# Kernel tuning notes

Hardware: AMD Instinct MI355X
Metric: run time of the kernel (lower is better)

## Reference

```python
import jax, jax.numpy as jnp
import numpy as np

E, B, T, N, DIN = 8, 1024, 64, 16, 8
H, Z = 512, 128
DFLAT = T * N * DIN  # 8192


def setup_inputs() -> dict:
    key = jax.random.key(0)
    ks = jax.random.split(key, 10)
    def w(k, shape, fan_in):
        return jax.random.normal(k, shape, jnp.float32) * (1.0 / np.sqrt(fan_in))
    return {
        'x': jax.random.normal(ks[0], (B, T, N, DIN), jnp.float32),
        'eps': jax.random.normal(ks[1], (E, B, Z), jnp.float32),
        'enc_w1': w(ks[2], (E, DFLAT, H), DFLAT), 'enc_b1': jnp.zeros((E, H), jnp.float32),
        'enc_w2': w(ks[3], (E, H, H), H),         'enc_b2': jnp.zeros((E, H), jnp.float32),
        'mu_w':   w(ks[4], (E, H, Z), H),         'mu_b':   jnp.zeros((E, Z), jnp.float32),
        'lv_w':   w(ks[5], (E, H, Z), H),         'lv_b':   jnp.zeros((E, Z), jnp.float32),
        'dec_w1': w(ks[6], (E, Z, H), Z),         'dec_b1': jnp.zeros((E, H), jnp.float32),
        'dec_w2': w(ks[7], (E, H, H), H),         'dec_b2': jnp.zeros((E, H), jnp.float32),
        'dec_w3': w(ks[8], (E, H, DFLAT), H),     'dec_b3': jnp.zeros((E, DFLAT), jnp.float32),
    }


def _all_experts(x, eps, enc_w1, enc_b1, enc_w2, enc_b2, mu_w, mu_b, lv_w, lv_b,
                 dec_w1, dec_b1, dec_w2, dec_b2, dec_w3, dec_b3):
    # 'everyone_try_this_problem': every expert runs densely on the full batch.
    xf = x.reshape(x.shape[0], -1)                                            # [B, D]
    h = jax.nn.relu(jnp.einsum('bd,edh->ebh', xf, enc_w1) + enc_b1[:, None])  # [E, B, H]
    h = jax.nn.relu(jnp.einsum('ebh,ehk->ebk', h, enc_w2) + enc_b2[:, None])
    mu = jnp.einsum('ebh,ehz->ebz', h, mu_w) + mu_b[:, None]                  # [E, B, Z]
    logvar = jnp.einsum('ebh,ehz->ebz', h, lv_w) + lv_b[:, None]
    z = mu + jnp.exp(0.5 * logvar) * eps                                      # reparameterized sample
    hd = jax.nn.relu(jnp.einsum('ebz,ezh->ebh', z, dec_w1) + dec_b1[:, None])
    hd = jax.nn.relu(jnp.einsum('ebh,ehk->ebk', hd, dec_w2) + dec_b2[:, None])
    xhat = jnp.einsum('ebh,ehd->ebd', hd, dec_w3) + dec_b3[:, None]           # [E, B, D]
    losses = jnp.mean((xhat - xf[None]) ** 2, axis=-1)                        # [E, B] per-sample recon loss
    return mu, logvar, xhat, losses


def reference(x, eps, enc_w1, enc_b1, enc_w2, enc_b2, mu_w, mu_b, lv_w, lv_b,
              dec_w1, dec_b1, dec_w2, dec_b2, dec_w3, dec_b3):
    mu, logvar, xhat, losses = _all_experts(
        x, eps, enc_w1, enc_b1, enc_w2, enc_b2, mu_w, mu_b, lv_w, lv_b,
        dec_w1, dec_b1, dec_w2, dec_b2, dec_w3, dec_b3)
    # torch.min(all_loss[B,E], dim=1) -> argmin over experts (first-index tiebreak)
    expert_idx = jnp.argmin(losses, axis=0)                                   # [B]
    b = jnp.arange(x.shape[0])
    mu_sel = mu[expert_idx, b]                                                # [B, Z]
    logvar_sel = logvar[expert_idx, b]
    xhat_sel = xhat[expert_idx, b].reshape(x.shape)                           # [B, T, N, DIN]
    return mu_sel, logvar_sel, xhat_sel, expert_idx
```

## Files before the change

kernel.cpp:

```cpp
#include <hip/hip_runtime.h>

#define EE 8
#define BB 1024
#define DD 8192
#define HH 512
#define ZZ 128

typedef __attribute__((ext_vector_type(8))) short bf16x8;
typedef __attribute__((ext_vector_type(4))) float f32x4;
typedef __attribute__((address_space(1))) unsigned int u32g;
typedef __attribute__((address_space(3))) unsigned int u32l;

#define DEVI __device__ __forceinline__

DEVI float4 ld4(const float* p) { return *(const float4*)p; }

DEVI unsigned f2bf_u(float x) {
  unsigned u = __builtin_bit_cast(unsigned, x);
  return (u + 0x7FFFu + ((u >> 16) & 1u)) >> 16;
}
DEVI float bfu2f(unsigned h) { return __builtin_bit_cast(float, h << 16); }
DEVI float bf2f(short s) {
  return __builtin_bit_cast(float, ((unsigned)(unsigned short)s) << 16);
}
DEVI void split2(float x, short& hi, short& lo) {
  unsigned h = f2bf_u(x);
  hi = (short)h;
  lo = (short)f2bf_u(x - bfu2f(h));
}

DEVI void gload16(const void* g, void* l) {
  __builtin_amdgcn_global_load_lds((const u32g*)g, (u32l*)l, 16, 0, 0);
}

DEVI void pipe_fence() {
  __builtin_amdgcn_sched_barrier(0);
  asm volatile("s_waitcnt vmcnt(0)" ::: "memory");
  __builtin_amdgcn_s_barrier();
  __builtin_amdgcn_sched_barrier(0);
}

template <int ROWS, int WAVES>
DEVI void stageG(const short* src, int Kb, short* lds, int w, int laneoff) {
  const char* p = (const char*)src + laneoff;
  char* l = (char*)lds + w * 1024;
#pragma unroll
  for (int r = 0; r < ROWS / (WAVES * 8); ++r)
    gload16(p + (size_t)r * (WAVES * 8) * Kb, l + r * (WAVES * 1024));
}

template <int ROWS, int WAVES>
DEVI void stage32(const short* src, int Kb, short* lds, int w, int laneoff32) {
  const char* p = (const char*)src + laneoff32;
  char* l = (char*)lds + w * 1024;
#pragma unroll
  for (int r = 0; r < ROWS / (WAVES * 16); ++r)
    gload16(p + (size_t)r * (WAVES * 16) * Kb, l + r * (WAVES * 1024));
}

template <int NPASS, int NF>
DEVI void mma_chunk(const char* Ah, const char* Al, const char* Bh, const char* Bl,
                    int abase, int bbase, f32x4 acc[4][NF]) {
#pragma unroll
  for (int kk = 0; kk < 2; ++kk) {
    const int kx = kk * 64;
    bf16x8 ah[4], al[4], bh[NF], bl[NF];
#pragma unroll
    for (int m = 0; m < 4; ++m) {
      ah[m] = *(const bf16x8*)(Ah + ((abase + m * 2048) ^ kx));
      if (NPASS == 3) al[m] = *(const bf16x8*)(Al + ((abase + m * 2048) ^ kx));
    }
#pragma unroll
    for (int n = 0; n < NF; ++n) {
      bh[n] = *(const bf16x8*)(Bh + ((bbase + n * 2048) ^ kx));
      if (NPASS == 3) bl[n] = *(const bf16x8*)(Bl + ((bbase + n * 2048) ^ kx));
    }
#pragma unroll
    for (int m = 0; m < 4; ++m)
#pragma unroll
      for (int n = 0; n < NF; ++n) {
        acc[m][n] = __builtin_amdgcn_mfma_f32_16x16x32_bf16(ah[m], bh[n], acc[m][n], 0, 0, 0);
        if (NPASS == 3) {
          acc[m][n] = __builtin_amdgcn_mfma_f32_16x16x32_bf16(ah[m], bl[n], acc[m][n], 0, 0, 0);
          acc[m][n] = __builtin_amdgcn_mfma_f32_16x16x32_bf16(al[m], bh[n], acc[m][n], 0, 0, 0);
        }
      }
  }
}

template <int NM, int NF>
DEVI void mma32(const char* A, const char* B, int abase, int bbase,
                f32x4 acc[NM][NF]) {
  bf16x8 ah[NM], bh[NF];
#pragma unroll
  for (int m = 0; m < NM; ++m) ah[m] = *(const bf16x8*)(A + abase + m * 1024);
#pragma unroll
  for (int n = 0; n < NF; ++n) bh[n] = *(const bf16x8*)(B + bbase + n * 1024);
#pragma unroll
  for (int m = 0; m < NM; ++m)
#pragma unroll
    for (int n = 0; n < NF; ++n)
      acc[m][n] = __builtin_amdgcn_mfma_f32_16x16x32_bf16(ah[m], bh[n], acc[m][n], 0, 0, 0);
}

template <int NPASS, int NF, bool RELU, int OUT>
__global__ __launch_bounds__(256, (NPASS == 3 ? 2 : 3)) void gemm_k(
    const short* __restrict__ Ahg, const short* __restrict__ Alg,
    const short* __restrict__ Bhg, const short* __restrict__ Blg,
    const float* __restrict__ bias,
    float* __restrict__ Yf, short* __restrict__ Yh, short* __restrict__ Yl,
    int M, int N, int K, int APE, const int* __restrict__ cntPtr, int mSkip) {
  constexpr int BN = NF * 32;
  __shared__ short sA[(NPASS == 3 ? 2 : 1) * 128 * 64];
  __shared__ short sB[(NPASS == 3 ? 2 : 1) * BN * 64];
  const int e = blockIdx.z;
  const int m0 = blockIdx.y * 128, n0 = blockIdx.x * BN;
  if (m0 < mSkip) return;
  if (cntPtr) {
    if (m0 >= ((cntPtr[0] + 127) & ~127)) return;
  }
  const size_t eA = APE ? (size_t)e * M * K : 0;
  const short* Ae = Ahg + eA + (size_t)m0 * K;
  const short* Ale = (NPASS == 3) ? (Alg + eA + (size_t)m0 * K) : nullptr;
  const short* Be = Bhg + ((size_t)e * N + n0) * K;
  const short* Ble = (NPASS == 3) ? (Blg + ((size_t)e * N + n0) * K) : nullptr;

  const int t = threadIdx.x, w = t >> 6, lane = t & 63;
  const int wm = w >> 1, wn = w & 1;
  const int Kb = K * 2;
  const int laneoff = (w * 8 + (lane >> 3)) * Kb + (((lane & 7) ^ ((lane >> 3) & 7)) << 4);
  const int r16 = lane & 15, g = lane >> 4;
  const int c0 = ((g ^ (r16 & 7)) << 4);
  const int abase = (wm * 64 + r16) * 128 + c0;
  const int bbase = (wn * (NF * 16) + r16) * 128 + c0;

  f32x4 acc[4][NF];
#pragma unroll
  for (int m = 0; m < 4; ++m)
#pragma unroll
    for (int n = 0; n < NF; ++n) acc[m][n] = (f32x4){0.f, 0.f, 0.f, 0.f};

  for (int k0 = 0; k0 < K; k0 += 64) {
    stageG<128, 4>(Ae + k0, Kb, sA, w, laneoff);
    if (NPASS == 3) stageG<128, 4>(Ale + k0, Kb, sA + 128 * 64, w, laneoff);
    stageG<BN, 4>(Be + k0, Kb, sB, w, laneoff);
    if (NPASS == 3) stageG<BN, 4>(Ble + k0, Kb, sB + BN * 64, w, laneoff);
    __syncthreads();
    mma_chunk<NPASS, NF>((const char*)sA, (const char*)(sA + 128 * 64),
                         (const char*)sB, (const char*)(sB + BN * 64), abase, bbase, acc);
    __syncthreads();
  }

  const int col0 = n0 + wn * (NF * 16);
#pragma unroll
  for (int n = 0; n < NF; ++n) {
    const int cn = col0 + n * 16 + r16;
    const float bv = bias[(size_t)e * N + cn];
#pragma unroll
    for (int m = 0; m < 4; ++m)
#pragma unroll
      for (int r = 0; r < 4; ++r) {
        const int row = m0 + wm * 64 + m * 16 + g * 4 + r;
        float v = acc[m][n][r] + bv;
        if (RELU) v = fmaxf(v, 0.f);
        const size_t o = ((size_t)e * M + row) * N + cn;
        if (OUT == 0) {
          Yf[o] = v;
        } else {
          unsigned hb = f2bf_u(v);
          Yh[o] = (short)hb;
          if (NPASS == 3) Yl[o] = (short)f2bf_u(v - bfu2f(hb));
        }
      }
  }
}

__global__ __launch_bounds__(256, 4) void enc1_mainsplit_k(
    const short* __restrict__ Xhg, const short* __restrict__ Bhg,
    float* __restrict__ EncP) {
  __shared__ short sA[2][128 * 32];
  __shared__ short sB[2][64 * 32];
  const int raw = blockIdx.x;
  const int e = raw & 7;
  const int q = raw >> 3;
  const int m0 = (q & 7) * 128;
  const int ks = (q >> 3) & 1;
  const int n0 = (q >> 4) * 64;
  const int Kb = DD * 2;
  const short* Ae = Xhg + (size_t)m0 * DD;
  const short* Be = Bhg + ((size_t)e * HH + n0) * DD;

  const int t = threadIdx.x, w = t >> 6, lane = t & 63;
  const int wm = w >> 1, wn = w & 1;
  const int lo32 = (w * 16 + (lane >> 2)) * Kb +
                   (((lane & 3) ^ ((lane >> 3) & 3)) << 4);
  const int r16 = lane & 15, g = lane >> 4;
  const int c32 = (g ^ ((r16 >> 1) & 3)) << 4;
  const int abase = (wm * 64 + r16) * 64 + c32;
  const int bbase = (wn * 32 + r16) * 64 + c32;

  f32x4 acc[4][2];
#pragma unroll
  for (int m = 0; m < 4; ++m)
#pragma unroll
    for (int n = 0; n < 2; ++n) acc[m][n] = (f32x4){0.f, 0.f, 0.f, 0.f};

  const int kbeg = ks * 4096;
  stage32<128, 4>(Ae + kbeg, Kb, sA[0], w, lo32);
  stage32<64, 4>(Be + kbeg, Kb, sB[0], w, lo32);
  pipe_fence();
  for (int c = 0; c < 128; c += 2) {
    if (c + 1 < 128) {
      stage32<128, 4>(Ae + kbeg + (c + 1) * 32, Kb, sA[1], w, lo32);
      stage32<64, 4>(Be + kbeg + (c + 1) * 32, Kb, sB[1], w, lo32);
    }
    mma32<4, 2>((const char*)sA[0], (const char*)sB[0], abase, bbase, acc);
    pipe_fence();
    if (c + 2 < 128) {
      stage32<128, 4>(Ae + kbeg + (c + 2) * 32, Kb, sA[0], w, lo32);
      stage32<64, 4>(Be + kbeg + (c + 2) * 32, Kb, sB[0], w, lo32);
    }
    mma32<4, 2>((const char*)sA[1], (const char*)sB[1], abase, bbase, acc);
    pipe_fence();
  }

#pragma unroll
  for (int n = 0; n < 2; ++n) {
    const int cn = n0 + wn * 32 + n * 16 + r16;
#pragma unroll
    for (int m = 0; m < 4; ++m)
#pragma unroll
      for (int r = 0; r < 4; ++r) {
        const int row = m0 + wm * 64 + m * 16 + g * 4 + r;
        EncP[(((size_t)ks * EE + e) * BB + row) * HH + cn] = acc[m][n][r];
      }
  }
}

__global__ void fuse_enc1main_k(const float* __restrict__ EncP,
                                const float* __restrict__ enc_b1,
                                short* __restrict__ Hh) {
  const int idx = blockIdx.x * 256 + threadIdx.x;
  const size_t base = (size_t)idx * 8;
  float s[8];
  *(float4*)&s[0] = *(const float4*)&EncP[base];
  *(float4*)&s[4] = *(const float4*)&EncP[base + 4];
  {
    const float* p = EncP + (size_t)(EE * BB * HH) + base;
    float q[8];
    *(float4*)&q[0] = *(const float4*)p;
    *(float4*)&q[4] = *(const float4*)(p + 4);
#pragma unroll
    for (int j = 0; j < 8; ++j) s[j] += q[j];
  }
  const int e = (int)(base / (BB * HH));
  const int col = (int)(base % HH);
  short h8[8];
#pragma unroll
  for (int j = 0; j < 8; ++j) {
    const float v = fmaxf(s[j] + enc_b1[e * HH + col + j], 0.f);
    h8[j] = (short)f2bf_u(v);
  }
  *(bf16x8*)&Hh[base] = *(bf16x8*)h8;
}

__global__ __launch_bounds__(512, 2) void gemm_loss256_k(
    const short* __restrict__ Ahg, const short* __restrict__ Bhg,
    const float* __restrict__ bias, const short* __restrict__ xfh,
    float* __restrict__ partials) {
  __shared__ short sA[2][256 * 32];
  __shared__ short sB[2][256 * 32];
  __shared__ float red[256][4];
  int lin = blockIdx.x + 32 * (blockIdx.y + 4 * blockIdx.z);
  lin = (lin & 7) * 128 + (lin >> 3);
  const int bx = lin & 31, by = (lin >> 5) & 3, e = lin >> 7;
  const int m0 = by * 256, n0 = bx * 256;
  const int Kb = HH * 2;
  const short* Ae = Ahg + ((size_t)e * BB + m0) * HH;
  const short* Be = Bhg + ((size_t)e * DD + n0) * HH;

  const int t = threadIdx.x, w = t >> 6, lane = t & 63;
  const int wm = w >> 2, wn = w & 3;
  const int lo32 = (w * 16 + (lane >> 2)) * Kb +
                   (((lane & 3) ^ ((lane >> 3) & 3)) << 4);
  const int r16 = lane & 15, g = lane >> 4;
  const int c32 = (g ^ ((r16 >> 1) & 3)) << 4;
  const int abase = (wm * 128 + r16) * 64 + c32;
  const int bbase = (wn * 64 + r16) * 64 + c32;

  f32x4 acc[8][4];
#pragma unroll
  for (int m = 0; m < 8; ++m)
#pragma unroll
    for (int n = 0; n < 4; ++n) acc[m][n] = (f32x4){0.f, 0.f, 0.f, 0.f};

  stage32<256, 8>(Ae, Kb, sA[0], w, lo32);
  stage32<256, 8>(Be, Kb, sB[0], w, lo32);
  pipe_fence();
  for (int c = 0; c < 16; c += 2) {
    if (c + 1 < 16) {
      stage32<256, 8>(Ae + (c + 1) * 32, Kb, sA[1], w, lo32);
      stage32<256, 8>(Be + (c + 1) * 32, Kb, sB[1], w, lo32);
    }
    mma32<8, 4>((const char*)sA[0], (const char*)sB[0], abase, bbase, acc);
    pipe_fence();
    if (c + 2 < 16) {
      stage32<256, 8>(Ae + (c + 2) * 32, Kb, sA[0], w, lo32);
      stage32<256, 8>(Be + (c + 2) * 32, Kb, sB[0], w, lo32);
    }
    mma32<8, 4>((const char*)sA[1], (const char*)sB[1], abase, bbase, acc);
    pipe_fence();
  }

  float rs[8][4];
#pragma unroll
  for (int m = 0; m < 8; ++m)
#pragma unroll
    for (int r = 0; r < 4; ++r) rs[m][r] = 0.f;
#pragma unroll
  for (int n = 0; n < 4; ++n) {
    const int cn = n0 + wn * 64 + n * 16 + r16;
    const float bv = bias[(size_t)e * DD + cn];
#pragma unroll
    for (int m = 0; m < 8; ++m)
#pragma unroll
      for (int r = 0; r < 4; ++r) {
        const int row = m0 + wm * 128 + m * 16 + g * 4 + r;
        const float d = acc[m][n][r] + bv - bf2f(xfh[(size_t)row * DD + cn]);
        rs[m][r] = fmaf(d, d, rs[m][r]);
      }
  }
#pragma unroll
  for (int off = 1; off < 16; off <<= 1)
#pragma unroll
    for (int m = 0; m < 8; ++m)
#pragma unroll
      for (int r = 0; r < 4; ++r) rs[m][r] += __shfl_xor(rs[m][r], off);
  if (r16 == 0) {
#pragma unroll
    for (int m = 0; m < 8; ++m)
#pragma unroll
      for (int r = 0; r < 4; ++r) red[wm * 128 + m * 16 + g * 4 + r][wn] = rs[m][r];
  }
  __syncthreads();
  if (t < 256)
    partials[((size_t)e * BB + m0 + t) * 32 + bx] =
        red[t][0] + red[t][1] + red[t][2] + red[t][3];
}

template <int NPASS>
__global__ __launch_bounds__(256, 2) void gemm_loss_k(
    const short* __restrict__ Ahg, const short* __restrict__ Alg,
    const short* __restrict__ Bhg, const short* __restrict__ Blg,
    const float* __restrict__ bias, const float* __restrict__ xf,
    const int* __restrict__ rows, const int* __restrict__ cntPtr,
    float* __restrict__ partials, int K) {
  constexpr int NF = 4;
  __shared__ short sA[2 * 128 * 64];
  __shared__ short sB[2 * 128 * 64];
  __shared__ float red[128][2];
  const int e = blockIdx.z;
  const int m0 = blockIdx.y * 128, n0 = blockIdx.x * 128;
  int cntA = BB;
  if (cntPtr) {
    cntA = cntPtr[0];
    if (m0 >= ((cntA + 127) & ~127)) return;
  }
  const short* Ae = Ahg + ((size_t)e * BB + m0) * K;
  const short* Ale = Alg + ((size_t)e * BB + m0) * K;
  const short* Be = Bhg + ((size_t)e * DD + n0) * K;
  const short* Ble = Blg + ((size_t)e * DD + n0) * K;

  const int t = threadIdx.x, w = t >> 6, lane = t & 63;
  const int wm = w >> 1, wn = w & 1;
  const int Kb = K * 2;
  const int laneoff = (w * 8 + (lane >> 3)) * Kb + (((lane & 7) ^ ((lane >> 3) & 7)) << 4);
  const int r16 = lane & 15, g = lane >> 4;
  const int c0 = ((g ^ (r16 & 7)) << 4);
  const int abase = (wm * 64 + r16) * 128 + c0;
  const int bbase = (wn * 64 + r16) * 128 + c0;

  f32x4 acc[4][NF];
#pragma unroll
  for (int m = 0; m < 4; ++m)
#pragma unroll
    for (int n = 0; n < NF; ++n) acc[m][n] = (f32x4){0.f, 0.f, 0.f, 0.f};

  for (int k0 = 0; k0 < K; k0 += 64) {
    stageG<128, 4>(Ae + k0, Kb, sA, w, laneoff);
    stageG<128, 4>(Ale + k0, Kb, sA + 128 * 64, w, laneoff);
    stageG<128, 4>(Be + k0, Kb, sB, w, laneoff);
    stageG<128, 4>(Ble + k0, Kb, sB + 128 * 64, w, laneoff);
    __syncthreads();
    mma_chunk<NPASS, NF>((const char*)sA, (const char*)(sA + 128 * 64),
                         (const char*)sB, (const char*)(sB + 128 * 64), abase, bbase, acc);
    __syncthreads();
  }

  float rs[4][4];
#pragma unroll
  for (int m = 0; m < 4; ++m)
#pragma unroll
    for (int r = 0; r < 4; ++r) rs[m][r] = 0.f;
#pragma unroll
  for (int n = 0; n < NF; ++n) {
    const int cn = n0 + wn * 64 + n * 16 + r16;
    const float bv = bias[(size_t)e * DD + cn];
#pragma unroll
    for (int m = 0; m < 4; ++m)
#pragma unroll
      for (int r = 0; r < 4; ++r) {
        const int lrow = m0 + wm * 64 + m * 16 + g * 4 + r;
        const int xr = rows ? (lrow < cntA ? rows[lrow] : 0) : lrow;
        const float d = acc[m][n][r] + bv - xf[(size_t)xr * DD + cn];
        rs[m][r] = fmaf(d, d, rs[m][r]);
      }
  }
#pragma unroll
  for (int off = 1; off < 16; off <<= 1)
#pragma unroll
    for (int m = 0; m < 4; ++m)
#pragma unroll
      for (int r = 0; r < 4; ++r) rs[m][r] += __shfl_xor(rs[m][r], off);
  if (r16 == 0) {
#pragma unroll
    for (int m = 0; m < 4; ++m)
#pragma unroll
      for (int r = 0; r < 4; ++r) red[wm * 64 + m * 16 + g * 4 + r][wn] = rs[m][r];
  }
  __syncthreads();
  if (t < 128)
    partials[((size_t)e * BB + m0 + t) * 64 + blockIdx.x] = red[t][0] + red[t][1];
}

__global__ __launch_bounds__(512, 2) void gather_out256_k(
    const short* __restrict__ Ahg, const short* __restrict__ Bhg,
    const float* __restrict__ bias, const int* __restrict__ counts,
    const int* __restrict__ lists, float* __restrict__ out) {
  __shared__ short sA[2][256 * 32];
  __shared__ short sB[2][256 * 32];
  __shared__ int rows_s[256];
  const int e = blockIdx.z;
  const int cnt = counts[e];
  const int m0 = blockIdx.y * 256;
  if (m0 >= cnt) return;
  const int n0 = blockIdx.x * 256;
  const int Kb = HH * 2;
  const short* Ae = Ahg + (size_t)e * BB * HH;
  const short* Be = Bhg + ((size_t)e * DD + n0) * HH;

  const int t = threadIdx.x, w = t >> 6, lane = t & 63;
  const int wm = w >> 2, wn = w & 3;
  const int soff = ((lane & 3) ^ ((lane >> 3) & 3)) << 4;
  const int lo32 = (w * 16 + (lane >> 2)) * Kb + soff;
  const int r16 = lane & 15, g = lane >> 4;
  const int c32 = (g ^ ((r16 >> 1) & 3)) << 4;
  const int abase = (wm * 128 + r16) * 64 + c32;
  const int bbase = (wn * 64 + r16) * 64 + c32;

  if (t < 256) rows_s[t] = (m0 + t < cnt) ? lists[e * BB + m0 + t] : -1;
  __syncthreads();
  const int r1 = w * 16 + (lane >> 2), r2 = r1 + 128;
  int g1 = rows_s[r1]; g1 = g1 < 0 ? 0 : g1;
  int g2 = rows_s[r2]; g2 = g2 < 0 ? 0 : g2;

  f32x4 acc[8][4];
#pragma unroll
  for (int m = 0; m < 8; ++m)
#pragma unroll
    for (int n = 0; n < 4; ++n) acc[m][n] = (f32x4){0.f, 0.f, 0.f, 0.f};

  auto STAGE_A = [&](int ke, short* dst) {
    gload16((const char*)Ae + (size_t)g1 * Kb + (size_t)ke * 2 + soff,
            (char*)dst + w * 1024);
    gload16((const char*)Ae + (size_t)g2 * Kb + (size_t)ke * 2 + soff,
            (char*)dst + 8192 + w * 1024);
  };

  STAGE_A(0, sA[0]);
  stage32<256, 8>(Be, Kb, sB[0], w, lo32);
  pipe_fence();
  for (int c = 0; c < 16; c += 2) {
    if (c + 1 < 16) {
      STAGE_A((c + 1) * 32, sA[1]);
      stage32<256, 8>(Be + (c + 1) * 32, Kb, sB[1], w, lo32);
    }
    mma32<8, 4>((const char*)sA[0], (const char*)sB[0], abase, bbase, acc);
    pipe_fence();
    if (c + 2 < 16) {
      STAGE_A((c + 2) * 32, sA[0]);
      stage32<256, 8>(Be + (c + 2) * 32, Kb, sB[0], w, lo32);
    }
    mma32<8, 4>((const char*)sA[1], (const char*)sB[1], abase, bbase, acc);
    pipe_fence();
  }

#pragma unroll
  for (int n = 0; n < 4; ++n) {
    const int cn = n0 + wn * 64 + n * 16 + r16;
    const float bv = bias[(size_t)e * DD + cn];
#pragma unroll
    for (int m = 0; m < 8; ++m)
#pragma unroll
      for (int r = 0; r < 4; ++r) {
        const int rout = rows_s[wm * 128 + m * 16 + g * 4 + r];
        if (rout >= 0) out[(size_t)rout * DD + cn] = acc[m][n][r] + bv;
      }
  }
}

__global__ __launch_bounds__(256, 2) void enc1_pksplit_k(
    const short* __restrict__ Ahg, const short* __restrict__ Alg,
    const short* __restrict__ Bhg, const short* __restrict__ Blg,
    const int* __restrict__ cntPtr, float* __restrict__ PAf) {
  __shared__ short sA[2 * 128 * 64];
  __shared__ short sB[2 * 64 * 64];
  const int cnt = cntPtr[0];
  if (cnt == 0) return;
  const int m0 = blockIdx.y * 128;
  if (m0 >= ((cnt + 127) & ~127)) return;
  const int e = blockIdx.z;
  const int n0 = (blockIdx.x & 7) * 64;
  const int ks = blockIdx.x >> 3;
  const int Kb = DD * 2;
  const short* Ae = Ahg + (size_t)m0 * DD;
  const short* Ale = Alg + (size_t)m0 * DD;
  const short* Be = Bhg + ((size_t)e * HH + n0) * DD;
  const short* Ble = Blg + ((size_t)e * HH + n0) * DD;

  const int t = threadIdx.x, w = t >> 6, lane = t & 63;
  const int wm = w >> 1, wn = w & 1;
  const int laneoff = (w * 8 + (lane >> 3)) * Kb + (((lane & 7) ^ ((lane >> 3) & 7)) << 4);
  const int r16 = lane & 15, g = lane >> 4;
  const int c0 = ((g ^ (r16 & 7)) << 4);
  const int abase = (wm * 64 + r16) * 128 + c0;
  const int bbase = (wn * 32 + r16) * 128 + c0;

  f32x4 acc[4][2];
#pragma unroll
  for (int m = 0; m < 4; ++m)
#pragma unroll
    for (int n = 0; n < 2; ++n) acc[m][n] = (f32x4){0.f, 0.f, 0.f, 0.f};

  const int kbeg = ks * 1024, kend = kbeg + 1024;
  for (int k0 = kbeg; k0 < kend; k0 += 64) {
    stageG<128, 4>(Ae + k0, Kb, sA, w, laneoff);
    stageG<128, 4>(Ale + k0, Kb, sA + 128 * 64, w, laneoff);
    stageG<64, 4>(Be + k0, Kb, sB, w, laneoff);
    stageG<64, 4>(Ble + k0, Kb, sB + 64 * 64, w, laneoff);
    __syncthreads();
    mma_chunk<3, 2>((const char*)sA, (const char*)(sA + 128 * 64),
                    (const char*)sB, (const char*)(sB + 64 * 64), abase, bbase, acc);
    __syncthreads();
  }

#pragma unroll
  for (int n = 0; n < 2; ++n) {
    const int cn = n0 + wn * 32 + n * 16 + r16;
#pragma unroll
    for (int m = 0; m < 4; ++m)
#pragma unroll
      for (int r = 0; r < 4; ++r) {
        const int row = m0 + wm * 64 + m * 16 + g * 4 + r;
        PAf[(((size_t)ks * EE + e) * 256 + row) * HH + cn] = acc[m][n][r];
      }
  }
}

__global__ void fuse_enc1_k(const float* __restrict__ PAf,
                            const float* __restrict__ enc_b1,
                            const int* __restrict__ ambc,
                            short* __restrict__ PAh, short* __restrict__ PAl) {
  const int cnt = ambc[0];
  if (cnt == 0) return;
  const int cntPad = (cnt + 127) & ~127;
  const int idx = blockIdx.x * 256 + threadIdx.x;
  const size_t base = (size_t)idx * 8;
  const int e = (int)(base / (256 * HH));
  const int rem = (int)(base % (256 * HH));
  const int row = rem / HH;
  if (row >= cntPad) return;
  const int col = rem % HH;
  const size_t src = ((size_t)e * 256 + row) * HH + col;
  float s[8];
  *(float4*)&s[0] = *(const float4*)&PAf[src];
  *(float4*)&s[4] = *(const float4*)&PAf[src + 4];
#pragma unroll
  for (int ks = 1; ks < 8; ++ks) {
    const float* p = PAf + (size_t)ks * (EE * 256 * HH) + src;
    float q[8];
    *(float4*)&q[0] = *(const float4*)p;
    *(float4*)&q[4] = *(const float4*)(p + 4);
#pragma unroll
    for (int j = 0; j < 8; ++j) s[j] += q[j];
  }
  short h8[8], l8[8];
#pragma unroll
  for (int j = 0; j < 8; ++j) {
    const float v = fmaxf(s[j] + enc_b1[e * HH + col + j], 0.f);
    split2(v, h8[j], l8[j]);
  }
  const size_t o = ((size_t)e * BB + row) * HH + col;
  *(bf16x8*)&PAh[o] = *(bf16x8*)h8;
  *(bf16x8*)&PAl[o] = *(bf16x8*)l8;
}

__global__ void init_k(int* ambc) { ambc[0] = 0; }

__global__ void split_x_k(const float* __restrict__ x, short* __restrict__ Xh) {
  const int i = (blockIdx.x * 256 + threadIdx.x) * 8;
  float v[8];
  *(float4*)&v[0] = ld4(x + i);
  *(float4*)&v[4] = ld4(x + i + 4);
  short h[8];
#pragma unroll
  for (int j = 0; j < 8; ++j) h[j] = (short)f2bf_u(v[j]);
  *(bf16x8*)&Xh[i] = *(bf16x8*)h;
}

__global__ void biascat_k(const float* __restrict__ mu_b, const float* __restrict__ lv_b,
                          float* __restrict__ mlvB) {
  const int e = blockIdx.x, t = threadIdx.x;
  mlvB[e * 256 + t] = t < 128 ? mu_b[e * 128 + t] : lv_b[e * 128 + t - 128];
}

__global__ __launch_bounds__(256) void trans_split_k(
    const float* __restrict__ W, short* __restrict__ Th, short* __restrict__ Tl,
    int K, int N, int rowOff, int rowsPerE) {
  const int e = blockIdx.z;
  const int k0 = blockIdx.x * 64, n0 = blockIdx.y * 64;
  __shared__ float tile[64][65];
  const int t = threadIdx.x;
  const int tr = t >> 2, tc = (t & 3) * 16;
  const float* Wp = W + ((size_t)e * K + k0 + tr) * N + n0 + tc;
#pragma unroll
  for (int c = 0; c < 4; ++c) {
    float4 v = *(const float4*)(Wp + c * 4);
    tile[tr][tc + c * 4 + 0] = v.x;
    tile[tr][tc + c * 4 + 1] = v.y;
    tile[tr][tc + c * 4 + 2] = v.z;
    tile[tr][tc + c * 4 + 3] = v.w;
  }
  __syncthreads();
  short h8[16], l8[16];
#pragma unroll
  for (int j = 0; j < 16; ++j) split2(tile[tc + j][tr], h8[j], l8[j]);
  const size_t o = ((size_t)e * rowsPerE + rowOff + n0 + tr) * K + k0 + tc;
  *(bf16x8*)&Th[o] = *(bf16x8*)&h8[0];
  *(bf16x8*)&Th[o + 8] = *(bf16x8*)&h8[8];
  *(bf16x8*)&Tl[o] = *(bf16x8*)&l8[0];
  *(bf16x8*)&Tl[o + 8] = *(bf16x8*)&l8[8];
}

__global__ void z_k(const float* __restrict__ mlv, const float* __restrict__ eps,
                    short* __restrict__ Zh) {
  const int t = blockIdx.x * 256 + threadIdx.x;
  const int eb = t >> 7, z = t & 127;
  const float mu = mlv[(size_t)eb * 256 + z], lv = mlv[(size_t)eb * 256 + 128 + z];
  Zh[t] = (short)f2bf_u(fmaf(expf(0.5f * lv), eps[t], mu));
}

__global__ void zP_k(const float* __restrict__ mlvP, const float* __restrict__ eps,
                     const int* __restrict__ ambc, const int* __restrict__ amb,
                     short* __restrict__ ZgH, short* __restrict__ ZgL) {
  const int t = blockIdx.x * 256 + threadIdx.x;
  const int eb = t >> 7, z = t & 127;
  const int e = eb >> 10, i = eb & 1023;
  const int cntA = ambc[0];
  if (i >= ((cntA + 127) & ~127)) return;
  const int b = (i < cntA) ? amb[i] : 0;
  const float mu = mlvP[(size_t)eb * 256 + z], lv = mlvP[(size_t)eb * 256 + 128 + z];
  const float v = fmaf(expf(0.5f * lv), eps[((size_t)e * BB + b) * ZZ + z], mu);
  short h, l;
  split2(v, h, l);
  ZgH[t] = h;
  ZgL[t] = l;
}

__global__ void gather_x_k(const float* __restrict__ x, const int* __restrict__ ambc,
                           const int* __restrict__ amb, short* __restrict__ XgH,
                           short* __restrict__ XgL) {
  const int i = blockIdx.x;
  const int cntA = ambc[0];
  if (i >= ((cntA + 127) & ~127)) return;
  const int b = (i < cntA) ? amb[i] : 0;
  const float* xr = x + (size_t)b * DD;
  short* oh = XgH + (size_t)i * DD;
  short* ol = XgL + (size_t)i * DD;
  for (int j = threadIdx.x * 8; j < DD; j += 256 * 8) {
    float v[8];
    *(float4*)&v[0] = ld4(xr + j);
    *(float4*)&v[4] = ld4(xr + j + 4);
    short h[8], l[8];
#pragma unroll
    for (int q = 0; q < 8; ++q) split2(v[q], h[q], l[q]);
    *(bf16x8*)&oh[j] = *(bf16x8*)h;
    *(bf16x8*)&ol[j] = *(bf16x8*)l;
  }
}

__global__ void loss_reduce_k(const float* __restrict__ part, float* __restrict__ loss,
                              const int* __restrict__ cntPtr, int NBLK) {
  const int id = blockIdx.x * 256 + threadIdx.x;
  if (cntPtr) {
    if ((id & 1023) >= ((cntPtr[0] + 127) & ~127)) return;
  }
  const float* p = part + (size_t)id * NBLK;
  float s = 0.f;
  for (int j = 0; j < NBLK; ++j) s += p[j];
  loss[id] = s;
}

__global__ void argmin_flag_k(const float* __restrict__ loss, int* __restrict__ idx,
                              float* __restrict__ out_ix, int* __restrict__ ambc,
                              int* __restrict__ amb) {
  const int b = blockIdx.x * 256 + threadIdx.x;
  float best = loss[b], sec = 3.0e38f;
  int bi = 0;
#pragma unroll
  for (int e = 1; e < EE; ++e) {
    const float v = loss[e * BB + b];
    if (v < best) { sec = best; best = v; bi = e; }
    else if (v < sec) sec = v;
  }
  idx[b] = bi;
  out_ix[b] = (float)bi;
  if (sec - best < 10.0f + 0.001f * best) {
    int p = atomicAdd(ambc, 1);
    amb[p] = b;
  }
}

__global__ void fix_idx_k(const float* __restrict__ lossP, const int* __restrict__ ambc,
                          const int* __restrict__ amb, int* __restrict__ idx,
                          float* __restrict__ out_ix) {
  const int i = blockIdx.x * 256 + threadIdx.x;
  if (i >= ambc[0]) return;
  const int b = amb[i];
  float best = lossP[i];
  int bi = 0;
#pragma unroll
  for (int e = 1; e < EE; ++e) {
    const float v = lossP[e * 1024 + i];
    if (v < best) { best = v; bi = e; }
  }
  idx[b] = bi;
  out_ix[b] = (float)bi;
}

__global__ void select_k(const float* __restrict__ mlv, const int* __restrict__ idx,
                         float* __restrict__ out_mu, float* __restrict__ out_lv) {
  const int t = blockIdx.x * 256 + threadIdx.x;
  const int b = t >> 7, z = t & 127;
  const int e = idx[b];
  out_mu[t] = mlv[((size_t)(e * BB + b)) * 256 + z];
  out_lv[t] = mlv[((size_t)(e * BB + b)) * 256 + 128 + z];
}

__global__ void compact_k(const int* __restrict__ idx, int* __restrict__ counts,
                          int* __restrict__ lists) {
  __shared__ int cnt[EE];
  if (threadIdx.x < EE) cnt[threadIdx.x] = 0;
  __syncthreads();
  const int b = threadIdx.x;
  const int e = idx[b];
  const int pos = atomicAdd(&cnt[e], 1);
  lists[e * BB + pos] = b;
  __syncthreads();
  if (threadIdx.x < EE) counts[threadIdx.x] = cnt[threadIdx.x];
}

extern "C" void kernel_launch(void* const* d_in, const int* in_sizes, int n_in,
                              void* d_out, int out_size, void* d_ws, size_t ws_size,
                              hipStream_t stream) {
  const float* x      = (const float*)d_in[0];
  const float* eps    = (const float*)d_in[1];
  const float* enc_w1 = (const float*)d_in[2];
  const float* enc_b1 = (const float*)d_in[3];
  const float* enc_w2 = (const float*)d_in[4];
  const float* enc_b2 = (const float*)d_in[5];
  const float* mu_w   = (const float*)d_in[6];
  const float* mu_b   = (const float*)d_in[7];
  const float* lv_w   = (const float*)d_in[8];
  const float* lv_b   = (const float*)d_in[9];
  const float* dec_w1 = (const float*)d_in[10];
  const float* dec_b1 = (const float*)d_in[11];
  const float* dec_w2 = (const float*)d_in[12];
  const float* dec_b2 = (const float*)d_in[13];
  const float* dec_w3 = (const float*)d_in[14];
  const float* dec_b3 = (const float*)d_in[15];

  char* wsb = (char*)d_ws;
  size_t off = 0;
  auto alloc = [&](size_t bytes) -> void* {
    void* p = wsb + off;
    off = (off + bytes + 511) & ~(size_t)511;
    return p;
  };
  short* Xh    = (short*)alloc(16777216);
  short* ew1Th = (short*)alloc(67108864);
  short* ew1Tl = (short*)alloc(67108864);
  short* ew2Th = (short*)alloc(4194304);
  short* ew2Tl = (short*)alloc(4194304);
  short* mlvTh = (short*)alloc(2097152);
  short* mlvTl = (short*)alloc(2097152);
  short* dw1Th = (short*)alloc(1048576);
  short* dw1Tl = (short*)alloc(1048576);
  short* dw2Th = (short*)alloc(4194304);
  short* dw2Tl = (short*)alloc(4194304);
  short* dw3Th = (short*)alloc(67108864);
  short* dw3Tl = (short*)alloc(67108864);
  short* Hh    = (short*)alloc(8388608);
  short* H2h   = (short*)alloc(8388608);
  float* mlv   = (float*)alloc(8388608);
  float* mlvB  = (float*)alloc(8192);
  short* Zh    = (short*)alloc(2097152);
  float* part  = (float*)alloc(2097152);
  float* loss  = (float*)alloc(32768);
  int*   idx   = (int*)alloc(4096);
  int*   ambc  = (int*)alloc(512);
  int*   amb   = (int*)alloc(4096);
  int*   counts= (int*)alloc(512);
  int*   lists = (int*)alloc(4096);
  short* XgL   = (short*)alloc(16777216);
  short* PAh   = (short*)alloc(8388608);
  short* PAl   = (short*)alloc(8388608);
  short* PBh   = (short*)alloc(8388608);
  short* PBl   = (short*)alloc(8388608);
  float* mlvP  = (float*)alloc(8388608);
  short* ZgH   = (short*)alloc(2097152);
  short* ZgL   = (short*)alloc(2097152);
  float* lossP = (float*)alloc(32768);
  float* PAf   = (float*)alloc(33554432);
  short* XgH   = Xh;
  float* EncP  = (float*)XgL;

  float* out_mu = (float*)d_out;
  float* out_lv = out_mu + (size_t)BB * ZZ;
  float* out_xh = out_lv + (size_t)BB * ZZ;
  float* out_ix = out_xh + (size_t)BB * DD;

  const dim3 blk(256);

  init_k<<<1, 1, 0, stream>>>(ambc);
  split_x_k<<<4096, blk, 0, stream>>>(x, Xh);
  biascat_k<<<8, blk, 0, stream>>>(mu_b, lv_b, mlvB);
  trans_split_k<<<dim3(128, 8, 8), blk, 0, stream>>>(enc_w1, ew1Th, ew1Tl, 8192, 512, 0, 512);
  trans_split_k<<<dim3(8, 8, 8), blk, 0, stream>>>(enc_w2, ew2Th, ew2Tl, 512, 512, 0, 512);
  trans_split_k<<<dim3(8, 2, 8), blk, 0, stream>>>(mu_w, mlvTh, mlvTl, 512, 128, 0, 256);
  trans_split_k<<<dim3(8, 2, 8), blk, 0, stream>>>(lv_w, mlvTh, mlvTl, 512, 128, 128, 256);
  trans_split_k<<<dim3(2, 8, 8), blk, 0, stream>>>(dec_w1, dw1Th, dw1Tl, 128, 512, 0, 512);
  trans_split_k<<<dim3(8, 8, 8), blk, 0, stream>>>(dec_w2, dw2Th, dw2Tl, 512, 512, 0, 512);
  trans_split_k<<<dim3(8, 128, 8), blk, 0, stream>>>(dec_w3, dw3Th, dw3Tl, 512, 8192, 0, 8192);

  enc1_mainsplit_k<<<dim3(1024), blk, 0, stream>>>(Xh, ew1Th, EncP);
  fuse_enc1main_k<<<2048, blk, 0, stream>>>(EncP, enc_b1, Hh);
  gemm_k<1, 2, true, 1><<<dim3(8, 8, 8), blk, 0, stream>>>(
      Hh, nullptr, ew2Th, nullptr, enc_b2, nullptr, H2h, nullptr, 1024, 512, 512, 1, nullptr, 0);
  gemm_k<1, 2, false, 0><<<dim3(4, 8, 8), blk, 0, stream>>>(
      H2h, nullptr, mlvTh, nullptr, mlvB, mlv, nullptr, nullptr, 1024, 256, 512, 1, nullptr, 0);
  z_k<<<4096, blk, 0, stream>>>(mlv, eps, Zh);
  gemm_k<1, 2, true, 1><<<dim3(8, 8, 8), blk, 0, stream>>>(
      Zh, nullptr, dw1Th, nullptr, dec_b1, nullptr, Hh, nullptr, 1024, 512, 128, 1, nullptr, 0);
  gemm_k<1, 2, true, 1><<<dim3(8, 8, 8), blk, 0, stream>>>(
      Hh, nullptr, dw2Th, nullptr, dec_b2, nullptr, H2h, nullptr, 1024, 512, 512, 1, nullptr, 0);
  gemm_loss256_k<<<dim3(32, 4, 8), dim3(512), 0, stream>>>(
      H2h, dw3Th, dec_b3, Xh, part);
  loss_reduce_k<<<32, blk, 0, stream>>>(part, loss, nullptr, 32);
  argmin_flag_k<<<4, blk, 0, stream>>>(loss, idx, out_ix, ambc, amb);

  gather_x_k<<<1024, blk, 0, stream>>>(x, ambc, amb, XgH, XgL);
  enc1_pksplit_k<<<dim3(64, 2, 8), blk, 0, stream>>>(
      XgH, XgL, ew1Th, ew1Tl, ambc, PAf);
  fuse_enc1_k<<<512, blk, 0, stream>>>(PAf, enc_b1, ambc, PAh, PAl);
  gemm_k<3, 2, true, 1><<<dim3(8, 8, 8), blk, 0, stream>>>(
      XgH, XgL, ew1Th, ew1Tl, enc_b1, nullptr, PAh, PAl, 1024, 512, 8192, 0, ambc, 256);
  gemm_k<3, 2, true, 1><<<dim3(8, 8, 8), blk, 0, stream>>>(
      PAh, PAl, ew2Th, ew2Tl, enc_b2, nullptr, PBh, PBl, 1024, 512, 512, 1, ambc, 0);
  gemm_k<3, 2, false, 0><<<dim3(4, 8, 8), blk, 0, stream>>>(
      PBh, PBl, mlvTh, mlvTl, mlvB, mlvP, nullptr, nullptr, 1024, 256, 512, 1, ambc, 0);
  zP_k<<<4096, blk, 0, stream>>>(mlvP, eps, ambc, amb, ZgH, ZgL);
  gemm_k<3, 2, true, 1><<<dim3(8, 8, 8), blk, 0, stream>>>(
      ZgH, ZgL, dw1Th, dw1Tl, dec_b1, nullptr, PAh, PAl, 1024, 512, 128, 1, ambc, 0);
  gemm_k<3, 2, true, 1><<<dim3(8, 8, 8), blk, 0, stream>>>(
      PAh, PAl, dw2Th, dw2Tl, dec_b2, nullptr, PBh, PBl, 1024, 512, 512, 1, ambc, 0);
  gemm_loss_k<3><<<dim3(64, 8, 8), blk, 0, stream>>>(
      PBh, PBl, dw3Th, dw3Tl, dec_b3, x, amb, ambc, part, 512);
  loss_reduce_k<<<32, blk, 0, stream>>>(part, lossP, ambc, 64);
  fix_idx_k<<<4, blk, 0, stream>>>(lossP, ambc, amb, idx, out_ix);

  select_k<<<512, blk, 0, stream>>>(mlv, idx, out_mu, out_lv);
  compact_k<<<1, 1024, 0, stream>>>(idx, counts, lists);
  gather_out256_k<<<dim3(32, 4, 8), dim3(512), 0, stream>>>(
      H2h, dw3Th, dec_b3, counts, lists, out_xh);
}
```

Measured before the change: 652.7 us.

## Enlarge enc1 split-K tile to 128x128 with single-buffered 64-wide K chunks

The encoder first-layer split-K kernel now computes a 128x128 output tile per block instead of 128x64, halving the grid to 512 blocks and doubling operand reuse per staged tile. It also drops the double-buffered 32-wide K pipeline in favour of a single 64-wide chunk staged with the generic stageG/mma_chunk helpers, guarded by two __syncthreads per iteration. This is meant to reduce redundant global loads of X and weights, but it gives up load/compute overlap and raises accumulator registers, which may cut occupancy.

Result: faster. 630.4 us (median of 2 runs) (-3.4%).

```diff
diff --git a/kernel.cpp b/kernel.cpp
--- a/kernel.cpp
+++ b/kernel.cpp
@@ -178,55 +178,45 @@
 __global__ __launch_bounds__(256, 4) void enc1_mainsplit_k(
     const short* __restrict__ Xhg, const short* __restrict__ Bhg,
     float* __restrict__ EncP) {
-  __shared__ short sA[2][128 * 32];
-  __shared__ short sB[2][64 * 32];
+  __shared__ short sA[128 * 64];
+  __shared__ short sB[128 * 64];
   const int raw = blockIdx.x;
   const int e = raw & 7;
   const int q = raw >> 3;
   const int m0 = (q & 7) * 128;
   const int ks = (q >> 3) & 1;
-  const int n0 = (q >> 4) * 64;
+  const int n0 = (q >> 4) * 128;
   const int Kb = DD * 2;
   const short* Ae = Xhg + (size_t)m0 * DD;
   const short* Be = Bhg + ((size_t)e * HH + n0) * DD;
 
   const int t = threadIdx.x, w = t >> 6, lane = t & 63;
   const int wm = w >> 1, wn = w & 1;
-  const int lo32 = (w * 16 + (lane >> 2)) * Kb +
-                   (((lane & 3) ^ ((lane >> 3) & 3)) << 4);
+  const int laneoff = (w * 8 + (lane >> 3)) * Kb + (((lane & 7) ^ ((lane >> 3) & 7)) << 4);
   const int r16 = lane & 15, g = lane >> 4;
-  const int c32 = (g ^ ((r16 >> 1) & 3)) << 4;
-  const int abase = (wm * 64 + r16) * 64 + c32;
-  const int bbase = (wn * 32 + r16) * 64 + c32;
-
-  f32x4 acc[4][2];
+  const int c0 = ((g ^ (r16 & 7)) << 4);
+  const int abase = (wm * 64 + r16) * 128 + c0;
+  const int bbase = (wn * 64 + r16) * 128 + c0;
+
+  f32x4 acc[4][4];
 #pragma unroll
   for (int m = 0; m < 4; ++m)
 #pragma unroll
-    for (int n = 0; n < 2; ++n) acc[m][n] = (f32x4){0.f, 0.f, 0.f, 0.f};
-
-  const int kbeg = ks * 4096;
-  stage32<128, 4>(Ae + kbeg, Kb, sA[0], w, lo32);
-  stage32<64, 4>(Be + kbeg, Kb, sB[0], w, lo32);
-  pipe_fence();
-  for (int c = 0; c < 128; c += 2) {
-    if (c + 1 < 128) {
-      stage32<128, 4>(Ae + kbeg + (c + 1) * 32, Kb, sA[1], w, lo32);
-      stage32<64, 4>(Be + kbeg + (c + 1) * 32, Kb, sB[1], w, lo32);
-    }
-    mma32<4, 2>((const char*)sA[0], (const char*)sB[0], abase, bbase, acc);
-    pipe_fence();
-    if (c + 2 < 128) {
-      stage32<128, 4>(Ae + kbeg + (c + 2) * 32, Kb, sA[0], w, lo32);
-      stage32<64, 4>(Be + kbeg + (c + 2) * 32, Kb, sB[0], w, lo32);
-    }
-    mma32<4, 2>((const char*)sA[1], (const char*)sB[1], abase, bbase, acc);
-    pipe_fence();
-  }
-
-#pragma unroll
-  for (int n = 0; n < 2; ++n) {
-    const int cn = n0 + wn * 32 + n * 16 + r16;
+    for (int n = 0; n < 4; ++n) acc[m][n] = (f32x4){0.f, 0.f, 0.f, 0.f};
+
+  const int kbeg = ks * 4096, kend = kbeg + 4096;
+  for (int k0 = kbeg; k0 < kend; k0 += 64) {
+    stageG<128, 4>(Ae + k0, Kb, sA, w, laneoff);
+    stageG<128, 4>(Be + k0, Kb, sB, w, laneoff);
+    __syncthreads();
+    mma_chunk<1, 4>((const char*)sA, nullptr, (const char*)sB, nullptr,
+                    abase, bbase, acc);
+    __syncthreads();
+  }
+
+#pragma unroll
+  for (int n = 0; n < 4; ++n) {
+    const int cn = n0 + wn * 64 + n * 16 + r16;
 #pragma unroll
     for (int m = 0; m < 4; ++m)
 #pragma unroll
@@ -853,7 +843,7 @@
   trans_split_k<<<dim3(8, 8, 8), blk, 0, stream>>>(dec_w2, dw2Th, dw2Tl, 512, 512, 0, 512);
   trans_split_k<<<dim3(8, 128, 8), blk, 0, stream>>>(dec_w3, dw3Th, dw3Tl, 512, 8192, 0, 8192);
 
-  enc1_mainsplit_k<<<dim3(1024), blk, 0, stream>>>(Xh, ew1Th, EncP);
+  enc1_mainsplit_k<<<dim3(512), blk, 0, stream>>>(Xh, ew1Th, EncP);
   fuse_enc1main_k<<<2048, blk, 0, stream>>>(EncP, enc_b1, Hh);
   gemm_k<1, 2, true, 1><<<dim3(8, 8, 8), blk, 0, stream>>>(
       Hh, nullptr, ew2Th, nullptr, enc_b2, nullptr, H2h, nullptr, 1024, 512, 512, 1, nullptr, 0);
```
